# Optimization experiments

Hardware: AMD Instinct MI355X
Metric: run time of the kernel (lower is better)

The kernel has to match this reference:

```python
import jax, jax.numpy as jnp
import numpy as np

ALPHA, BETA, GAMMA, DELTA, EPSILON = 1.0, 0.15, 0.05, 0.0, 0.1
C1 = (0.01 * 255.0) ** 2
C2 = (0.03 * 255.0) ** 2


def _gaussian_kernel11():
    # cv2.getGaussianKernel(11, 1.5) outer product
    g = np.exp(-((np.arange(11) - 5.0) ** 2) / (2.0 * 1.5 ** 2))
    g = g / g.sum()
    return jnp.asarray(np.outer(g, g), dtype=jnp.float32)


def _to_uint8_float(x):
    # clamp to [-1,1], map to [0,1], scale to 255, uint8 truncation (floor)
    x = jnp.clip(x, -1.0, 1.0)
    x01 = jnp.clip((x + 1.0) * 0.5, 0.0, 1.0)
    return jnp.floor(jnp.clip(x01 * 255.0, 0.0, 255.0))


def _depthwise_valid_conv(x, kern2d):
    # x: [B,C,H,W]; 11x11 gaussian, VALID padding == filter2D + [5:-5,5:-5] crop
    C = x.shape[1]
    k = jnp.broadcast_to(kern2d[None, None], (C, 1, 11, 11))
    return jax.lax.conv_general_dilated(
        x, k, window_strides=(1, 1), padding='VALID',
        dimension_numbers=('NCHW', 'OIHW', 'NCHW'), feature_group_count=C)


def _ssim_per_image(img1, img2):
    # img1/img2: [B,C,H,W] floats in [0,255]; basicsr-style SSIM per channel, mean over C
    kern = _gaussian_kernel11()
    conv = lambda t: _depthwise_valid_conv(t, kern)
    mu1, mu2 = conv(img1), conv(img2)
    mu1_sq, mu2_sq, mu1_mu2 = mu1 * mu1, mu2 * mu2, mu1 * mu2
    sigma1_sq = conv(img1 * img1) - mu1_sq
    sigma2_sq = conv(img2 * img2) - mu2_sq
    sigma12 = conv(img1 * img2) - mu1_mu2
    ssim_map = ((2.0 * mu1_mu2 + C1) * (2.0 * sigma12 + C2)) / (
        (mu1_sq + mu2_sq + C1) * (sigma1_sq + sigma2_sq + C2))
    return jnp.mean(ssim_map, axis=(1, 2, 3))  # [B]


def _psnr_per_image(img1, img2):
    mse = jnp.mean((img1 - img2) ** 2, axis=(1, 2, 3))
    psnr = 10.0 * jnp.log10((255.0 ** 2) / jnp.maximum(mse, 1e-12))
    return jnp.where(mse == 0.0, 100.0, psnr)


def setup_inputs() -> dict:
    key = jax.random.key(0)
    k1, k2 = jax.random.split(key)
    shape = (4, 1, 2048, 2048)
    pred = jax.random.normal(k1, shape, dtype=jnp.float32) * 0.5
    target = jax.random.normal(k2, shape, dtype=jnp.float32) * 0.5
    return {"pred": pred, "target": target}


def reference(pred, target):
    # L1 loss
    l1 = jnp.mean(jnp.abs(pred - target))

    # edge-aware gradient loss (finite differences along H and W)
    gx = lambda t: t[:, :, :-1, :] - t[:, :, 1:, :]
    gy = lambda t: t[:, :, :, :-1] - t[:, :, :, 1:]
    grad_loss = (jnp.mean(jnp.abs(gx(pred) - gx(target))) +
                 jnp.mean(jnp.abs(gy(pred) - gy(target))))

    # physical consistency: per-image/channel mean & unbiased std stats + range penalty
    pm = jnp.mean(pred, axis=(2, 3))
    tm = jnp.mean(target, axis=(2, 3))
    energy = jnp.mean((pm - tm) ** 2)
    n = pred.shape[2] * pred.shape[3]
    ps = jnp.sqrt(jnp.sum((pred - pm[:, :, None, None]) ** 2, axis=(2, 3)) / (n - 1))
    ts = jnp.sqrt(jnp.sum((target - tm[:, :, None, None]) ** 2, axis=(2, 3)) / (n - 1))
    dist = jnp.mean((ps - ts) ** 2)
    range_pen = jnp.mean(jax.nn.relu(jnp.abs(pred) - 1.0))
    phys = energy + 0.5 * dist + 0.1 * range_pen

    # SSIM / PSNR on uint8-quantized [0,255] images (metric path, no gradient)
    p8 = _to_uint8_float(pred)
    t8 = _to_uint8_float(target)
    ssim_mean = jnp.clip(jnp.mean(_ssim_per_image(p8, t8)), 0.0, 1.0)
    psnr_mean = jnp.mean(_psnr_per_image(p8, t8))
    ssim_loss = 1.0 - ssim_mean

    total = (ALPHA * l1 + BETA * grad_loss + GAMMA * phys +
             EPSILON * jax.lax.stop_gradient(ssim_loss))
    return total, psnr_mean, ssim_mean
```

## Files before the change

### kernel.cpp

```cpp
#include <hip/hip_runtime.h>
#include <math.h>

#define HDIM 2048
#define WDIM 2048
#define NPIX (HDIM*WDIM)
#define OUTW 2038

#define C1F 6.5025f
#define C2F 58.5225f

constexpr int TH   = 64, TW = 32;
constexpr int IN_R = 80;
constexpr int IQ_S = 56;
constexpr int IQ_H = IN_R * IQ_S;
constexpr int HT_R = 80;
constexpr int HT_A = 32 * HT_R;
constexpr int NCH  = 4;
constexpr int NBLK = 8192;

struct GaussW { float g[11]; };

typedef _Float16 half8 __attribute__((ext_vector_type(8)));
typedef float    f32x4 __attribute__((ext_vector_type(4)));
typedef float    f32x2 __attribute__((ext_vector_type(2)));

__device__ __forceinline__ float quant_u8f(float x) {
    float c = __builtin_amdgcn_fmed3f(x, -1.0f, 1.0f);
    return truncf((c + 1.0f) * 127.5f);
}

__device__ __forceinline__ f32x2 quant2(f32x2 x) {
    f32x2 c = { __builtin_amdgcn_fmed3f(x.x, -1.0f, 1.0f),
                __builtin_amdgcn_fmed3f(x.y, -1.0f, 1.0f) };
    f32x2 v = (c + 1.0f) * 127.5f;
    return { truncf(v.x), truncf(v.y) };
}

__device__ __forceinline__ unsigned pk2(float a, float b) {
    return __builtin_bit_cast(unsigned, __builtin_amdgcn_cvt_pkrtz(a, b));
}

__global__ __launch_bounds__(256, 7) void amsr2_fused(
        const float* __restrict__ pred, const float* __restrict__ targ,
        float* __restrict__ pr, GaussW gw)
{
    __shared__ alignas(16) _Float16 Ubuf[NCH * HT_A];
    __shared__ float sred[16][10];
    _Float16* Iq = Ubuf;
    _Float16* Tg = Ubuf + 2 * IQ_H;

    const int b  = blockIdx.z;
    const int r0 = blockIdx.y * TH;
    const int c0 = blockIdx.x * TW;
    const float* pb = pred + (size_t)b * NPIX;
    const float* tb = targ + (size_t)b * NPIX;
    const bool interior = (blockIdx.y < 31) && (blockIdx.x < 63);

    if (threadIdx.x < 16) {
        int n = threadIdx.x;
#pragma unroll
        for (int i = 0; i < 16; ++i) ((unsigned*)Tg)[n * 16 + i] = 0u;
#pragma unroll
        for (int j = 0; j < 11; ++j) Tg[n * 32 + n + j] = (_Float16)gw.g[j];
    }

    float s0 = 0.f, s1 = 0.f, s2 = 0.f, s3 = 0.f, ssum = 0.f;
    f32x2 s4v = {0.f, 0.f}, s5v = {0.f, 0.f}, s6v = {0.f, 0.f},
          s7v = {0.f, 0.f}, s8v = {0.f, 0.f}, ssv = {0.f, 0.f};

    if (interior) {
#pragma unroll
        for (int i = 0; i < 2; ++i) {
            int item = threadIdx.x + i * 256;
            int r = item >> 3, d = item & 7;
            const float* prow = pb + (size_t)(r0 + r) * WDIM + (c0 + d * 4);
            const float* trow = tb + (size_t)(r0 + r) * WDIM + (c0 + d * 4);
            float4 a4 = *(const float4*)prow;
            float4 b4 = *(const float4*)trow;
            float4 ad = *(const float4*)(prow + WDIM);
            float4 bd = *(const float4*)(trow + WDIM);
            float p5 = prow[4], t5 = trow[4];

            f32x2 a01 = {a4.x, a4.y}, a23 = {a4.z, a4.w};
            f32x2 b01 = {b4.x, b4.y}, b23 = {b4.z, b4.w};
            f32x2 dd01 = a01 - b01, dd23 = a23 - b23;
            float dd4 = p5 - t5;
            f32x2 g01 = f32x2{ad.x, ad.y} - f32x2{bd.x, bd.y};
            f32x2 g23 = f32x2{ad.z, ad.w} - f32x2{bd.z, bd.w};

            s0 += fabsf(dd01.x); s0 += fabsf(dd01.y);
            s0 += fabsf(dd23.x); s0 += fabsf(dd23.y);
            s1 += fabsf(dd01.x - g01.x); s1 += fabsf(dd01.y - g01.y);
            s1 += fabsf(dd23.x - g23.x); s1 += fabsf(dd23.y - g23.y);
            s2 += fabsf(dd01.x - dd01.y); s2 += fabsf(dd01.y - dd23.x);
            s2 += fabsf(dd23.x - dd23.y); s2 += fabsf(dd23.y - dd4);
            s3 += fmaxf(fabsf(a4.x) - 1.0f, 0.0f);
            s3 += fmaxf(fabsf(a4.y) - 1.0f, 0.0f);
            s3 += fmaxf(fabsf(a4.z) - 1.0f, 0.0f);
            s3 += fmaxf(fabsf(a4.w) - 1.0f, 0.0f);
            s4v += a01; s4v += a23;
            s5v += b01; s5v += b23;
            s6v += a01 * a01; s6v += a23 * a23;
            s7v += b01 * b01; s7v += b23 * b23;
            f32x2 qp01 = quant2(a01), qp23 = quant2(a23);
            f32x2 qt01 = quant2(b01), qt23 = quant2(b23);
            f32x2 qd01 = qp01 - qt01, qd23 = qp23 - qt23;
            s8v += qd01 * qd01; s8v += qd23 * qd23;

            *(uint2*)&Iq[r * IQ_S + d * 4] =
                make_uint2(pk2(qp01.x, qp01.y), pk2(qp23.x, qp23.y));
            *(uint2*)&Iq[IQ_H + r * IQ_S + d * 4] =
                make_uint2(pk2(qt01.x, qt01.y), pk2(qt23.x, qt23.y));
        }
        {
            int h = threadIdx.x;
            int r = h >> 2, d = 8 + (h & 3);
            const float* prow = pb + (size_t)(r0 + r) * WDIM + (c0 + d * 4);
            const float* trow = tb + (size_t)(r0 + r) * WDIM + (c0 + d * 4);
            float4 a4 = *(const float4*)prow;
            float4 b4 = *(const float4*)trow;
            f32x2 qp01 = quant2(f32x2{a4.x, a4.y}), qp23 = quant2(f32x2{a4.z, a4.w});
            f32x2 qt01 = quant2(f32x2{b4.x, b4.y}), qt23 = quant2(f32x2{b4.z, b4.w});
            *(uint2*)&Iq[r * IQ_S + d * 4] =
                make_uint2(pk2(qp01.x, qp01.y), pk2(qp23.x, qp23.y));
            *(uint2*)&Iq[IQ_H + r * IQ_S + d * 4] =
                make_uint2(pk2(qt01.x, qt01.y), pk2(qt23.x, qt23.y));
        }
        if (threadIdx.x < 192) {
            int h = threadIdx.x;
            int rq = h / 12;
            int r = 64 + rq, d = h - rq * 12;
            const float* prow = pb + (size_t)(r0 + r) * WDIM + (c0 + d * 4);
            const float* trow = tb + (size_t)(r0 + r) * WDIM + (c0 + d * 4);
            float4 a4 = *(const float4*)prow;
            float4 b4 = *(const float4*)trow;
            f32x2 qp01 = quant2(f32x2{a4.x, a4.y}), qp23 = quant2(f32x2{a4.z, a4.w});
            f32x2 qt01 = quant2(f32x2{b4.x, b4.y}), qt23 = quant2(f32x2{b4.z, b4.w});
            *(uint2*)&Iq[r * IQ_S + d * 4] =
                make_uint2(pk2(qp01.x, qp01.y), pk2(qp23.x, qp23.y));
            *(uint2*)&Iq[IQ_H + r * IQ_S + d * 4] =
                make_uint2(pk2(qt01.x, qt01.y), pk2(qt23.x, qt23.y));
        }
    } else {
#pragma unroll
        for (int i = 0; i < 2; ++i) {
            int item = threadIdx.x + i * 256;
            int r = item >> 3, d = item & 7;
            int gr = r0 + r, gc = c0 + d * 4;
            const float* prow = pb + (size_t)gr * WDIM + gc;
            const float* trow = tb + (size_t)gr * WDIM + gc;
            float4 a4 = *(const float4*)prow;
            float4 b4 = *(const float4*)trow;
            bool down = gr < (HDIM - 1);
            bool hasR = (gc + 4) < WDIM;
            float4 z4 = make_float4(0.f, 0.f, 0.f, 0.f);
            float4 ad = down ? *(const float4*)(prow + WDIM) : z4;
            float4 bd = down ? *(const float4*)(trow + WDIM) : z4;
            float p5 = hasR ? prow[4] : 0.0f;
            float t5 = hasR ? trow[4] : 0.0f;
            float pv[4] = {a4.x, a4.y, a4.z, a4.w};
            float tv[4] = {b4.x, b4.y, b4.z, b4.w};
            float pd[4] = {ad.x, ad.y, ad.z, ad.w};
            float td[4] = {bd.x, bd.y, bd.z, bd.w};
            float qp[4], qt[4];
#pragma unroll
            for (int k = 0; k < 4; ++k) { qp[k] = quant_u8f(pv[k]); qt[k] = quant_u8f(tv[k]); }
#pragma unroll
            for (int k = 0; k < 4; ++k) {
                float av = pv[k], bv = tv[k];
                float dd = av - bv;
                s0 += fabsf(dd);
                s3 += fmaxf(fabsf(av) - 1.0f, 0.0f);
                s4v.x += av;  s5v.x += bv;
                s6v.x = fmaf(av, av, s6v.x);
                s7v.x = fmaf(bv, bv, s7v.x);
                if (down) s1 += fabsf(dd - (pd[k] - td[k]));
                float nr  = (k < 3) ? pv[k + 1] : p5;
                float nt2 = (k < 3) ? tv[k + 1] : t5;
                if (k < 3 || hasR) s2 += fabsf(dd - (nr - nt2));
                float qd = qp[k] - qt[k];
                s8v.x = fmaf(qd, qd, s8v.x);
            }
            *(uint2*)&Iq[r * IQ_S + d * 4] =
                make_uint2(pk2(qp[0], qp[1]), pk2(qp[2], qp[3]));
            *(uint2*)&Iq[IQ_H + r * IQ_S + d * 4] =
                make_uint2(pk2(qt[0], qt[1]), pk2(qt[2], qt[3]));
        }
#pragma unroll
        for (int ph = 0; ph < 2; ++ph) {
            int r, d;
            bool active = true;
            if (ph == 0) { int h = threadIdx.x; r = h >> 2; d = 8 + (h & 3); }
            else {
                int h = threadIdx.x;
                active = h < 192;
                int rq = h / 12;
                r = 64 + rq; d = h - rq * 12;
            }
            if (active) {
                int gr = r0 + r, gc = c0 + d * 4;
                bool rowok = gr < HDIM;
                const float* prow = pb + (size_t)gr * WDIM + gc;
                const float* trow = tb + (size_t)gr * WDIM + gc;
                float qp[4], qt[4];
                if (rowok && (gc + 3) < WDIM) {
                    float4 a4 = *(const float4*)prow;
                    float4 b4 = *(const float4*)trow;
                    qp[0]=quant_u8f(a4.x); qp[1]=quant_u8f(a4.y); qp[2]=quant_u8f(a4.z); qp[3]=quant_u8f(a4.w);
                    qt[0]=quant_u8f(b4.x); qt[1]=quant_u8f(b4.y); qt[2]=quant_u8f(b4.z); qt[3]=quant_u8f(b4.w);
                } else {
#pragma unroll
                    for (int k = 0; k < 4; ++k) {
                        bool ok = rowok && (gc + k) < WDIM;
                        qp[k] = ok ? quant_u8f(prow[k]) : 0.0f;
                        qt[k] = ok ? quant_u8f(trow[k]) : 0.0f;
                    }
                }
                *(uint2*)&Iq[r * IQ_S + d * 4] =
                    make_uint2(pk2(qp[0], qp[1]), pk2(qp[2], qp[3]));
                *(uint2*)&Iq[IQ_H + r * IQ_S + d * 4] =
                    make_uint2(pk2(qt[0], qt[1]), pk2(qt[2], qt[3]));
            }
        }
    }
    __syncthreads();

    const int lane = threadIdx.x & 63;
    const int wid  = threadIdx.x >> 6;
    const int q    = lane >> 4;
    const int ml   = lane & 15;
    const half8 gfrag = *(const half8*)&Tg[ml * 32 + q * 8];
    const f32x4 zero4 = {0.f, 0.f, 0.f, 0.f};
    const _Float16 hquart = (_Float16)0.25f;

    const int npos = (wid < 2) ? 3 : 2;
    half8 hap[3], hat[3];
#pragma unroll
    for (int i = 0; i < 3; ++i) {
        if (i < npos) {
            int pos = wid + i * 4;
            int rb = (pos >> 1) * 16;
            int cb = pos & 1;
            int base = (rb + ml) * IQ_S + cb * 16 + q * 8;
            hap[i] = *(const half8*)&Iq[base];
            hat[i] = *(const half8*)&Iq[IQ_H + base];
        }
    }
    __syncthreads();

#pragma unroll
    for (int i = 0; i < 3; ++i) {
        if (i < npos) {
            int pos = wid + i * 4;
            int rb = (pos >> 1) * 16;
            int cb = pos & 1;
            const half8 ap = hap[i];
            const half8 at = hat[i];
            half8 m2 = (ap * hquart) * ap;
            m2 = (at * hquart) * at + m2;
            f32x4 d0 = __builtin_amdgcn_mfma_f32_16x16x32_f16(ap,      gfrag, zero4, 0, 0, 0);
            f32x4 d1 = __builtin_amdgcn_mfma_f32_16x16x32_f16(at,      gfrag, zero4, 0, 0, 0);
            f32x4 d2 = __builtin_amdgcn_mfma_f32_16x16x32_f16(m2,      gfrag, zero4, 0, 0, 0);
            f32x4 d3 = __builtin_amdgcn_mfma_f32_16x16x32_f16(ap * at, gfrag, zero4, 0, 0, 0);
            int hb = (cb * 16 + ml) * HT_R + rb + q * 4;
            *(uint2*)&Ubuf[0 * HT_A + hb] = make_uint2(pk2(d0[0], d0[1]), pk2(d0[2], d0[3]));
            *(uint2*)&Ubuf[1 * HT_A + hb] = make_uint2(pk2(d1[0], d1[1]), pk2(d1[2], d1[3]));
            *(uint2*)&Ubuf[2 * HT_A + hb] = make_uint2(pk2(d2[0], d2[1]), pk2(d2[2], d2[3]));
            *(uint2*)&Ubuf[3 * HT_A + hb] = make_uint2(pk2(d3[0], d3[1]), pk2(d3[2], d3[3]));
        }
    }
    __syncthreads();

    const int th_ = min(TH, OUTW - r0);
    const int tw_ = min(TW, OUTW - c0);
    for (int vp = wid; vp < 8; vp += 4) {
        int rb2 = (vp >> 1) * 16;
        int cb2 = vp & 1;
        f32x4 acc[NCH];
#pragma unroll
        for (int arr = 0; arr < NCH; ++arr) {
            const half8 bf = *(const half8*)&Ubuf[arr * HT_A +
                                                  (cb2 * 16 + ml) * HT_R + rb2 + q * 8];
            acc[arr] = __builtin_amdgcn_mfma_f32_16x16x32_f16(gfrag, bf, zero4, 0, 0, 0);
        }
        if (interior) {
#pragma unroll
            for (int pp = 0; pp < 2; ++pp) {
                f32x2 mu1 = {acc[0][2*pp], acc[0][2*pp+1]};
                f32x2 mu2 = {acc[1][2*pp], acc[1][2*pp+1]};
                f32x2 h2  = {acc[2][2*pp], acc[2][2*pp+1]};
                f32x2 h12 = {acc[3][2*pp], acc[3][2*pp+1]};
                f32x2 mu12 = mu1 * mu2, mu1s = mu1 * mu1, mu2s = mu2 * mu2;
                f32x2 sg12 = h12 - mu12;
                f32x2 sgs  = 4.0f * h2 - mu1s - mu2s;
                f32x2 num = (2.0f * mu12 + C1F) * (2.0f * sg12 + C2F);
                f32x2 den = (mu1s + mu2s + C1F) * (sgs + C2F);
                f32x2 rp = { __builtin_amdgcn_rcpf(den.x),
                             __builtin_amdgcn_rcpf(den.y) };
                ssv += num * rp;
            }
        } else {
            int col = cb2 * 16 + ml;
#pragma unroll
            for (int reg = 0; reg < 4; ++reg) {
                int row = rb2 + q * 4 + reg;
                if (row < th_ && col < tw_) {
                    float mu1 = acc[0][reg], mu2 = acc[1][reg];
                    float h2  = acc[2][reg], h12 = acc[3][reg];
                    float mu1s = mu1 * mu1, mu2s = mu2 * mu2, mu12 = mu1 * mu2;
                    float sg12 = h12 - mu12;
                    float sgs  = 4.0f * h2 - mu1s - mu2s;
                    float num = (2.0f * mu12 + C1F) * (2.0f * sg12 + C2F);
                    float den = (mu1s + mu2s + C1F) * (sgs + C2F);
                    ssum += num * __builtin_amdgcn_rcpf(den);
                }
            }
        }
    }

    float st10[10];
    st10[0] = s0; st10[1] = s1; st10[2] = s2; st10[3] = s3;
    st10[4] = s4v.x + s4v.y; st10[5] = s5v.x + s5v.y;
    st10[6] = s6v.x + s6v.y; st10[7] = s7v.x + s7v.y;
    st10[8] = s8v.x + s8v.y; st10[9] = ssum + ssv.x + ssv.y;
#pragma unroll
    for (int c = 0; c < 10; ++c) {
        float v = st10[c];
        v += __shfl_xor(v, 8);
        v += __shfl_xor(v, 4);
        v += __shfl_xor(v, 2);
        v += __shfl_xor(v, 1);
        st10[c] = v;
    }
    if ((lane & 15) == 0) {
        int g = wid * 4 + (lane >> 4);
#pragma unroll
        for (int c = 0; c < 10; ++c) sred[g][c] = st10[c];
    }
    __syncthreads();
    if (threadIdx.x < 10) {
        int c = threadIdx.x;
        float t = 0.0f;
#pragma unroll
        for (int g = 0; g < 16; ++g) t += sred[g][c];
        int bid = ((b * 32) + blockIdx.y) * 64 + blockIdx.x;
        pr[c * NBLK + bid] = t;
    }
}

__global__ __launch_bounds__(256) void amsr2_final(
        const float* __restrict__ pr, float* __restrict__ out)
{
    __shared__ double seg[40];
    int wid = threadIdx.x >> 6, lane = threadIdx.x & 63;
    for (int sidx = wid; sidx < 40; sidx += 4) {
        int c = sidx >> 2, b = sidx & 3;
        const float* base = pr + c * NBLK + b * 2048;
        float4 v[8];
#pragma unroll
        for (int it = 0; it < 8; ++it)
            v[it] = *(const float4*)(base + (it * 64 + lane) * 4);
        double acc = 0.0;
#pragma unroll
        for (int it = 0; it < 8; ++it)
            acc += (double)v[it].x + (double)v[it].y + (double)v[it].z + (double)v[it].w;
        for (int off = 32; off > 0; off >>= 1) acc += __shfl_down(acc, off);
        if (lane == 0) seg[sidx] = acc;
    }
    __syncthreads();
    if (threadIdx.x != 0) return;
    const double n = (double)NPIX;
    double sum0 = 0, sum1 = 0, sum2 = 0, sum3 = 0;
    for (int b = 0; b < 4; ++b) {
        sum0 += seg[0*4+b]; sum1 += seg[1*4+b]; sum2 += seg[2*4+b]; sum3 += seg[3*4+b];
    }
    double l1   = sum0 / (4.0 * n);
    double grad = sum1 / (4.0 * 2047.0 * 2048.0) + sum2 / (4.0 * 2048.0 * 2047.0);
    double energy = 0.0, dist = 0.0, psnr_sum = 0.0, ssim_sum = 0.0;
    for (int b = 0; b < 4; ++b) {
        double Sp  = seg[4*4+b],  St  = seg[5*4+b];
        double Spp = seg[6*4+b],  Stt = seg[7*4+b];
        double Su8 = seg[8*4+b],  Sss = seg[9*4+b];
        double pm = Sp / n, tm = St / n;
        double dm = pm - tm; energy += dm * dm;
        double vp = (Spp - n * pm * pm) / (n - 1.0);
        double vt = (Stt - n * tm * tm) / (n - 1.0);
        double ps = sqrt(fmax(vp, 0.0)), ts = sqrt(fmax(vt, 0.0));
        double dd = ps - ts; dist += dd * dd;
        double mse = Su8 / n;
        double psnr = (mse == 0.0) ? 100.0 : 10.0 * log10(65025.0 / fmax(mse, 1e-12));
        psnr_sum += psnr;
        ssim_sum += Sss / ((double)OUTW * (double)OUTW);
    }
    energy *= 0.25; dist *= 0.25;
    double range_pen = sum3 / (4.0 * n);
    double phys = energy + 0.5 * dist + 0.1 * range_pen;
    double ssim_mean = fmin(fmax(ssim_sum * 0.25, 0.0), 1.0);
    double total = l1 + 0.15 * grad + 0.05 * phys + 0.1 * (1.0 - ssim_mean);
    out[0] = (float)total;
    out[1] = (float)(psnr_sum * 0.25);
    out[2] = (float)ssim_mean;
}

extern "C" void kernel_launch(void* const* d_in, const int* in_sizes, int n_in,
                              void* d_out, int out_size, void* d_ws, size_t ws_size,
                              hipStream_t stream)
{
    (void)in_sizes; (void)n_in; (void)out_size; (void)ws_size;
    const float* pred = (const float*)d_in[0];
    const float* targ = (const float*)d_in[1];
    float* out = (float*)d_out;
    float* pr  = (float*)d_ws;

    GaussW gw;
    {
        double e[11], sm = 0.0;
        for (int i = 0; i < 11; ++i) {
            double d = (double)(i - 5);
            e[i] = exp(-(d * d) / 4.5);
            sm += e[i];
        }
        for (int i = 0; i < 11; ++i) gw.g[i] = (float)(e[i] / sm);
    }

    amsr2_fused<<<dim3(64, 32, 4), 256, 0, stream>>>(pred, targ, pr, gw);
    amsr2_final<<<1, 256, 0, stream>>>(pr, out);
}
```

Before: 178.1 us.

## Split fused kernel into streaming stats pass and uint8-staged MFMA SSIM conv

Replaces the single fused tile kernel with a streaming pass that reads pred/target once in column strips, accumulates all loss statistics (reusing the previous row for vertical gradients), and writes uint8-quantized images to workspace. A second kernel reads the compact uint8 halo tiles and runs the separable Gaussian via MFMA to compute the SSIM sum. The aim is to avoid redundant float halo reads and lighten the fused kernel. The cost is an extra global write and read of 32 MB of quantized data plus an extra launch. When the workspace is too small it falls back to the old path.

```diff
diff --git a/kernel.cpp b/kernel.cpp
--- a/kernel.cpp
+++ b/kernel.cpp
@@ -10,12 +10,17 @@
 #define C2F 58.5225f
 
 constexpr int TH   = 64, TW = 32;
-constexpr int IN_R = 80;
-constexpr int IQ_S = 56;
-constexpr int IQ_H = IN_R * IQ_S;
 constexpr int HT_R = 80;
 constexpr int HT_A = 32 * HT_R;
 constexpr int NCH  = 4;
+constexpr int NBLK2 = 8192;
+constexpr int PR9  = 9 * 1024;
+constexpr size_t QBYTES = (size_t)8 * NPIX;
+constexpr size_t WS_NEEDED = QBYTES + (size_t)(PR9 + NBLK2) * 4;
+
+constexpr int IQ_S = 56;
+constexpr int IN_R = 80;
+constexpr int IQ_H = IN_R * IQ_S;
 constexpr int NBLK = 8192;
 
 struct GaussW { float g[11]; };
@@ -28,19 +33,332 @@
     float c = __builtin_amdgcn_fmed3f(x, -1.0f, 1.0f);
     return truncf((c + 1.0f) * 127.5f);
 }
-
 __device__ __forceinline__ f32x2 quant2(f32x2 x) {
     f32x2 c = { __builtin_amdgcn_fmed3f(x.x, -1.0f, 1.0f),
                 __builtin_amdgcn_fmed3f(x.y, -1.0f, 1.0f) };
     f32x2 v = (c + 1.0f) * 127.5f;
     return { truncf(v.x), truncf(v.y) };
 }
-
 __device__ __forceinline__ unsigned pk2(float a, float b) {
     return __builtin_bit_cast(unsigned, __builtin_amdgcn_cvt_pkrtz(a, b));
 }
-
-__global__ __launch_bounds__(256, 7) void amsr2_fused(
+__device__ __forceinline__ unsigned pack4_u8(const float* v) {
+#if __has_builtin(__builtin_amdgcn_cvt_pk_u8_f32)
+    unsigned r = 0;
+    r = __builtin_amdgcn_cvt_pk_u8_f32(v[0], 0, r);
+    r = __builtin_amdgcn_cvt_pk_u8_f32(v[1], 1, r);
+    r = __builtin_amdgcn_cvt_pk_u8_f32(v[2], 2, r);
+    r = __builtin_amdgcn_cvt_pk_u8_f32(v[3], 3, r);
+    return r;
+#else
+    return ((unsigned)(int)v[0]) | (((unsigned)(int)v[1]) << 8) |
+           (((unsigned)(int)v[2]) << 16) | (((unsigned)(int)v[3]) << 24);
+#endif
+}
+__device__ __forceinline__ half8 unpack_u8x8(unsigned lo, unsigned hi) {
+    union { unsigned u[4]; half8 h; } r;
+    r.u[0] = pk2((float)(lo & 0xffu),         (float)((lo >> 8)  & 0xffu));
+    r.u[1] = pk2((float)((lo >> 16) & 0xffu), (float)((lo >> 24) & 0xffu));
+    r.u[2] = pk2((float)(hi & 0xffu),         (float)((hi >> 8)  & 0xffu));
+    r.u[3] = pk2((float)((hi >> 16) & 0xffu), (float)((hi >> 24) & 0xffu));
+    return r.h;
+}
+
+__global__ __launch_bounds__(256, 6) void amsr2_stream(
+        const float* __restrict__ pred, const float* __restrict__ targ,
+        unsigned char* __restrict__ qbuf, float* __restrict__ pr)
+{
+    __shared__ float sred[16][9];
+    const int g   = blockIdx.x * 256 + threadIdx.x;
+    const int b   = g >> 16;
+    const int rem = g & 65535;
+    const int seg = rem >> 9;
+    const int cg  = rem & 511;
+    const int r_start = seg * 16;
+    const bool hasR = (cg != 511);
+
+    const float* pp = pred + (size_t)b * NPIX + (size_t)r_start * WDIM + cg * 4;
+    const float* tt = targ + (size_t)b * NPIX + (size_t)r_start * WDIM + cg * 4;
+    unsigned char* qo = qbuf + (size_t)(b * 2) * NPIX + (size_t)r_start * WDIM + cg * 4;
+
+    float s0 = 0.f, s1 = 0.f, s2 = 0.f, s3 = 0.f;
+    f32x2 s4v = {0,0}, s5v = {0,0}, s6v = {0,0}, s7v = {0,0}, s8v = {0,0};
+    f32x2 pd01 = {0,0}, pd23 = {0,0};
+
+#pragma unroll 4
+    for (int it = 0; it < 16; ++it) {
+        float4 a4 = *(const float4*)pp;
+        float4 b4 = *(const float4*)tt;
+        float p5 = 0.f, t5 = 0.f;
+        if (hasR) { p5 = pp[4]; t5 = tt[4]; }
+
+        f32x2 a01 = {a4.x, a4.y}, a23 = {a4.z, a4.w};
+        f32x2 b01 = {b4.x, b4.y}, b23 = {b4.z, b4.w};
+        f32x2 dd01 = a01 - b01, dd23 = a23 - b23;
+        float dd4 = p5 - t5;
+
+        s0 += fabsf(dd01.x); s0 += fabsf(dd01.y);
+        s0 += fabsf(dd23.x); s0 += fabsf(dd23.y);
+        if (it > 0) {
+            s1 += fabsf(pd01.x - dd01.x); s1 += fabsf(pd01.y - dd01.y);
+            s1 += fabsf(pd23.x - dd23.x); s1 += fabsf(pd23.y - dd23.y);
+        }
+        s2 += fabsf(dd01.x - dd01.y); s2 += fabsf(dd01.y - dd23.x);
+        s2 += fabsf(dd23.x - dd23.y);
+        if (hasR) s2 += fabsf(dd23.y - dd4);
+        s3 += fmaxf(fabsf(a4.x) - 1.0f, 0.0f);
+        s3 += fmaxf(fabsf(a4.y) - 1.0f, 0.0f);
+        s3 += fmaxf(fabsf(a4.z) - 1.0f, 0.0f);
+        s3 += fmaxf(fabsf(a4.w) - 1.0f, 0.0f);
+        s4v += a01; s4v += a23;
+        s5v += b01; s5v += b23;
+        s6v += a01 * a01; s6v += a23 * a23;
+        s7v += b01 * b01; s7v += b23 * b23;
+        f32x2 qp01 = quant2(a01), qp23 = quant2(a23);
+        f32x2 qt01 = quant2(b01), qt23 = quant2(b23);
+        f32x2 qd01 = qp01 - qt01, qd23 = qp23 - qt23;
+        s8v += qd01 * qd01; s8v += qd23 * qd23;
+        float qpv[4] = {qp01.x, qp01.y, qp23.x, qp23.y};
+        float qtv[4] = {qt01.x, qt01.y, qt23.x, qt23.y};
+        *(unsigned*)qo          = pack4_u8(qpv);
+        *(unsigned*)(qo + NPIX) = pack4_u8(qtv);
+
+        pd01 = dd01; pd23 = dd23;
+        pp += WDIM; tt += WDIM; qo += WDIM;
+    }
+    if (seg != 127) {
+        float4 a4 = *(const float4*)pp;
+        float4 b4 = *(const float4*)tt;
+        f32x2 dd01 = f32x2{a4.x, a4.y} - f32x2{b4.x, b4.y};
+        f32x2 dd23 = f32x2{a4.z, a4.w} - f32x2{b4.z, b4.w};
+        s1 += fabsf(pd01.x - dd01.x); s1 += fabsf(pd01.y - dd01.y);
+        s1 += fabsf(pd23.x - dd23.x); s1 += fabsf(pd23.y - dd23.y);
+    }
+
+    const int lane = threadIdx.x & 63;
+    const int wid  = threadIdx.x >> 6;
+    float st9[9] = {s0, s1, s2, s3,
+                    s4v.x + s4v.y, s5v.x + s5v.y,
+                    s6v.x + s6v.y, s7v.x + s7v.y, s8v.x + s8v.y};
+#pragma unroll
+    for (int c = 0; c < 9; ++c) {
+        float v = st9[c];
+        v += __shfl_xor(v, 8);
+        v += __shfl_xor(v, 4);
+        v += __shfl_xor(v, 2);
+        v += __shfl_xor(v, 1);
+        st9[c] = v;
+    }
+    if ((lane & 15) == 0) {
+        int gi = wid * 4 + (lane >> 4);
+#pragma unroll
+        for (int c = 0; c < 9; ++c) sred[gi][c] = st9[c];
+    }
+    __syncthreads();
+    if (threadIdx.x < 9) {
+        int c = threadIdx.x;
+        float t = 0.0f;
+#pragma unroll
+        for (int gi = 0; gi < 16; ++gi) t += sred[gi][c];
+        pr[c * 1024 + blockIdx.x] = t;
+    }
+}
+
+__global__ __launch_bounds__(256, 6) void amsr2_conv(
+        const unsigned char* __restrict__ qbuf, float* __restrict__ pr, GaussW gw)
+{
+    __shared__ alignas(16) _Float16 HT[NCH * HT_A];
+    __shared__ alignas(16) _Float16 Tg[16 * 32];
+    __shared__ float sredS[16];
+
+    const int b  = blockIdx.z;
+    const int r0 = blockIdx.y * TH;
+    const int c0 = blockIdx.x * TW;
+    const bool interior = (blockIdx.y < 31) && (blockIdx.x < 63);
+    const unsigned char* qb0 = qbuf + (size_t)(b * 2) * NPIX;
+
+    if (threadIdx.x < 16) {
+        int n = threadIdx.x;
+#pragma unroll
+        for (int i = 0; i < 16; ++i) ((unsigned*)Tg)[n * 16 + i] = 0u;
+#pragma unroll
+        for (int j = 0; j < 11; ++j) Tg[n * 32 + n + j] = (_Float16)gw.g[j];
+    }
+
+    const int lane = threadIdx.x & 63;
+    const int wid  = threadIdx.x >> 6;
+    const int q    = lane >> 4;
+    const int ml   = lane & 15;
+    const f32x4 zero4 = {0.f, 0.f, 0.f, 0.f};
+    const _Float16 hquart = (_Float16)0.25f;
+
+    const int npos = (wid < 2) ? 3 : 2;
+    uint2 fp[3], ft[3];
+#pragma unroll
+    for (int i = 0; i < 3; ++i) {
+        if (i < npos) {
+            int pos = wid + i * 4;
+            int rb = (pos >> 1) * 16;
+            int cb = pos & 1;
+            int gr = r0 + rb + ml;       if (gr > HDIM - 1) gr = HDIM - 1;
+            int gc = c0 + cb * 16 + q * 8; if (gc > WDIM - 8) gc = WDIM - 8;
+            size_t off = (size_t)gr * WDIM + gc;
+            fp[i] = *(const uint2*)(qb0 + off);
+            ft[i] = *(const uint2*)(qb0 + NPIX + off);
+        }
+    }
+    __syncthreads();
+
+    const half8 gfrag = *(const half8*)&Tg[ml * 32 + q * 8];
+
+#pragma unroll
+    for (int i = 0; i < 3; ++i) {
+        if (i < npos) {
+            int pos = wid + i * 4;
+            int rb = (pos >> 1) * 16;
+            int cb = pos & 1;
+            const half8 ap = unpack_u8x8(fp[i].x, fp[i].y);
+            const half8 at = unpack_u8x8(ft[i].x, ft[i].y);
+            half8 m2 = (ap * hquart) * ap;
+            m2 = (at * hquart) * at + m2;
+            f32x4 d0 = __builtin_amdgcn_mfma_f32_16x16x32_f16(ap,      gfrag, zero4, 0, 0, 0);
+            f32x4 d1 = __builtin_amdgcn_mfma_f32_16x16x32_f16(at,      gfrag, zero4, 0, 0, 0);
+            f32x4 d2 = __builtin_amdgcn_mfma_f32_16x16x32_f16(m2,      gfrag, zero4, 0, 0, 0);
+            f32x4 d3 = __builtin_amdgcn_mfma_f32_16x16x32_f16(ap * at, gfrag, zero4, 0, 0, 0);
+            int hb = (cb * 16 + ml) * HT_R + rb + q * 4;
+            *(uint2*)&HT[0 * HT_A + hb] = make_uint2(pk2(d0[0], d0[1]), pk2(d0[2], d0[3]));
+            *(uint2*)&HT[1 * HT_A + hb] = make_uint2(pk2(d1[0], d1[1]), pk2(d1[2], d1[3]));
+            *(uint2*)&HT[2 * HT_A + hb] = make_uint2(pk2(d2[0], d2[1]), pk2(d2[2], d2[3]));
+            *(uint2*)&HT[3 * HT_A + hb] = make_uint2(pk2(d3[0], d3[1]), pk2(d3[2], d3[3]));
+        }
+    }
+    __syncthreads();
+
+    float ssum = 0.0f;
+    f32x2 ssv = {0.f, 0.f};
+    const int th_ = min(TH, OUTW - r0);
+    const int tw_ = min(TW, OUTW - c0);
+    for (int vp = wid; vp < 8; vp += 4) {
+        int rb2 = (vp >> 1) * 16;
+        int cb2 = vp & 1;
+        f32x4 acc[NCH];
+#pragma unroll
+        for (int arr = 0; arr < NCH; ++arr) {
+            const half8 bf = *(const half8*)&HT[arr * HT_A +
+                                               (cb2 * 16 + ml) * HT_R + rb2 + q * 8];
+            acc[arr] = __builtin_amdgcn_mfma_f32_16x16x32_f16(gfrag, bf, zero4, 0, 0, 0);
+        }
+        if (interior) {
+#pragma unroll
+            for (int pp = 0; pp < 2; ++pp) {
+                f32x2 mu1 = {acc[0][2*pp], acc[0][2*pp+1]};
+                f32x2 mu2 = {acc[1][2*pp], acc[1][2*pp+1]};
+                f32x2 h2  = {acc[2][2*pp], acc[2][2*pp+1]};
+                f32x2 h12 = {acc[3][2*pp], acc[3][2*pp+1]};
+                f32x2 mu12 = mu1 * mu2, mu1s = mu1 * mu1, mu2s = mu2 * mu2;
+                f32x2 sg12 = h12 - mu12;
+                f32x2 sgs  = 4.0f * h2 - mu1s - mu2s;
+                f32x2 num = (2.0f * mu12 + C1F) * (2.0f * sg12 + C2F);
+                f32x2 den = (mu1s + mu2s + C1F) * (sgs + C2F);
+                f32x2 rp = { __builtin_amdgcn_rcpf(den.x),
+                             __builtin_amdgcn_rcpf(den.y) };
+                ssv += num * rp;
+            }
+        } else {
+            int col = cb2 * 16 + ml;
+#pragma unroll
+            for (int reg = 0; reg < 4; ++reg) {
+                int row = rb2 + q * 4 + reg;
+                if (row < th_ && col < tw_) {
+                    float mu1 = acc[0][reg], mu2 = acc[1][reg];
+                    float h2  = acc[2][reg], h12 = acc[3][reg];
+                    float mu1s = mu1 * mu1, mu2s = mu2 * mu2, mu12 = mu1 * mu2;
+                    float sg12 = h12 - mu12;
+                    float sgs  = 4.0f * h2 - mu1s - mu2s;
+                    float num = (2.0f * mu12 + C1F) * (2.0f * sg12 + C2F);
+                    float den = (mu1s + mu2s + C1F) * (sgs + C2F);
+                    ssum += num * __builtin_amdgcn_rcpf(den);
+                }
+            }
+        }
+    }
+
+    float v = ssum + ssv.x + ssv.y;
+    v += __shfl_xor(v, 8);
+    v += __shfl_xor(v, 4);
+    v += __shfl_xor(v, 2);
+    v += __shfl_xor(v, 1);
+    if ((lane & 15) == 0) sredS[wid * 4 + (lane >> 4)] = v;
+    __syncthreads();
+    if (threadIdx.x == 0) {
+        float t = 0.0f;
+#pragma unroll
+        for (int gi = 0; gi < 16; ++gi) t += sredS[gi];
+        int bid2 = ((b * 32) + blockIdx.y) * 64 + blockIdx.x;
+        pr[PR9 + bid2] = t;
+    }
+}
+
+__global__ __launch_bounds__(256) void amsr2_final2(
+        const float* __restrict__ pr, float* __restrict__ out)
+{
+    __shared__ double seg[40];
+    int wid = threadIdx.x >> 6, lane = threadIdx.x & 63;
+    for (int sidx = wid; sidx < 40; sidx += 4) {
+        double acc = 0.0;
+        if (sidx < 36) {
+            int c = sidx >> 2, bb = sidx & 3;
+            const float* base = pr + c * 1024 + bb * 256;
+            float4 v = *(const float4*)(base + lane * 4);
+            acc = (double)v.x + (double)v.y + (double)v.z + (double)v.w;
+        } else {
+            int bb = sidx - 36;
+            const float* base = pr + PR9 + bb * 2048;
+#pragma unroll
+            for (int it = 0; it < 8; ++it) {
+                float4 v = *(const float4*)(base + (it * 64 + lane) * 4);
+                acc += (double)v.x + (double)v.y + (double)v.z + (double)v.w;
+            }
+        }
+        for (int off = 32; off > 0; off >>= 1) acc += __shfl_down(acc, off);
+        if (lane == 0) seg[sidx] = acc;
+    }
+    __syncthreads();
+    if (threadIdx.x != 0) return;
+    const double n = (double)NPIX;
+    double sum0 = 0, sum1 = 0, sum2 = 0, sum3 = 0;
+    for (int b = 0; b < 4; ++b) {
+        sum0 += seg[0*4+b]; sum1 += seg[1*4+b]; sum2 += seg[2*4+b]; sum3 += seg[3*4+b];
+    }
+    double l1   = sum0 / (4.0 * n);
+    double grad = sum1 / (4.0 * 2047.0 * 2048.0) + sum2 / (4.0 * 2048.0 * 2047.0);
+    double energy = 0.0, dist = 0.0, psnr_sum = 0.0, ssim_sum = 0.0;
+    for (int b = 0; b < 4; ++b) {
+        double Sp  = seg[4*4+b],  St  = seg[5*4+b];
+        double Spp = seg[6*4+b],  Stt = seg[7*4+b];
+        double Su8 = seg[8*4+b],  Sss = seg[36+b];
+        double pm = Sp / n, tm = St / n;
+        double dm = pm - tm; energy += dm * dm;
+        double vp = (Spp - n * pm * pm) / (n - 1.0);
+        double vt = (Stt - n * tm * tm) / (n - 1.0);
+        double ps = sqrt(fmax(vp, 0.0)), ts = sqrt(fmax(vt, 0.0));
+        double dd = ps - ts; dist += dd * dd;
+        double mse = Su8 / n;
+        double psnr = (mse == 0.0) ? 100.0 : 10.0 * log10(65025.0 / fmax(mse, 1e-12));
+        psnr_sum += psnr;
+        ssim_sum += Sss / ((double)OUTW * (double)OUTW);
+    }
+    energy *= 0.25; dist *= 0.25;
+    double range_pen = sum3 / (4.0 * n);
+    double phys = energy + 0.5 * dist + 0.1 * range_pen;
+    double ssim_mean = fmin(fmax(ssim_sum * 0.25, 0.0), 1.0);
+    double total = l1 + 0.15 * grad + 0.05 * phys + 0.1 * (1.0 - ssim_mean);
+    out[0] = (float)total;
+    out[1] = (float)(psnr_sum * 0.25);
+    out[2] = (float)ssim_mean;
+}
+
+__global__ __launch_bounds__(256, 7) void amsr2_fused_fb(
         const float* __restrict__ pred, const float* __restrict__ targ,
         float* __restrict__ pr, GaussW gw)
 {
@@ -65,8 +383,7 @@
     }
 
     float s0 = 0.f, s1 = 0.f, s2 = 0.f, s3 = 0.f, ssum = 0.f;
-    f32x2 s4v = {0.f, 0.f}, s5v = {0.f, 0.f}, s6v = {0.f, 0.f},
-          s7v = {0.f, 0.f}, s8v = {0.f, 0.f}, ssv = {0.f, 0.f};
+    f32x2 s4v = {0,0}, s5v = {0,0}, s6v = {0,0}, s7v = {0,0}, s8v = {0,0}, ssv = {0,0};
 
     if (interior) {
 #pragma unroll
@@ -80,14 +397,12 @@
             float4 ad = *(const float4*)(prow + WDIM);
             float4 bd = *(const float4*)(trow + WDIM);
             float p5 = prow[4], t5 = trow[4];
-
             f32x2 a01 = {a4.x, a4.y}, a23 = {a4.z, a4.w};
             f32x2 b01 = {b4.x, b4.y}, b23 = {b4.z, b4.w};
             f32x2 dd01 = a01 - b01, dd23 = a23 - b23;
             float dd4 = p5 - t5;
             f32x2 g01 = f32x2{ad.x, ad.y} - f32x2{bd.x, bd.y};
             f32x2 g23 = f32x2{ad.z, ad.w} - f32x2{bd.z, bd.w};
-
             s0 += fabsf(dd01.x); s0 += fabsf(dd01.y);
             s0 += fabsf(dd23.x); s0 += fabsf(dd23.y);
             s1 += fabsf(dd01.x - g01.x); s1 += fabsf(dd01.y - g01.y);
@@ -106,7 +421,6 @@
             f32x2 qt01 = quant2(b01), qt23 = quant2(b23);
             f32x2 qd01 = qp01 - qt01, qd23 = qp23 - qt23;
             s8v += qd01 * qd01; s8v += qd23 * qd23;
-
             *(uint2*)&Iq[r * IQ_S + d * 4] =
                 make_uint2(pk2(qp01.x, qp01.y), pk2(qp23.x, qp23.y));
             *(uint2*)&Iq[IQ_H + r * IQ_S + d * 4] =
@@ -348,7 +662,7 @@
     }
 }
 
-__global__ __launch_bounds__(256) void amsr2_final(
+__global__ __launch_bounds__(256) void amsr2_final_fb(
         const float* __restrict__ pr, float* __restrict__ out)
 {
     __shared__ double seg[40];
@@ -406,11 +720,10 @@
                               void* d_out, int out_size, void* d_ws, size_t ws_size,
                               hipStream_t stream)
 {
-    (void)in_sizes; (void)n_in; (void)out_size; (void)ws_size;
+    (void)in_sizes; (void)n_in; (void)out_size;
     const float* pred = (const float*)d_in[0];
     const float* targ = (const float*)d_in[1];
     float* out = (float*)d_out;
-    float* pr  = (float*)d_ws;
 
     GaussW gw;
     {
@@ -423,6 +736,15 @@
         for (int i = 0; i < 11; ++i) gw.g[i] = (float)(e[i] / sm);
     }
 
-    amsr2_fused<<<dim3(64, 32, 4), 256, 0, stream>>>(pred, targ, pr, gw);
-    amsr2_final<<<1, 256, 0, stream>>>(pr, out);
-}
+    if (ws_size >= WS_NEEDED) {
+        unsigned char* qbuf = (unsigned char*)d_ws;
+        float* pr = (float*)((char*)d_ws + QBYTES);
+        amsr2_stream<<<dim3(1024, 1, 1), 256, 0, stream>>>(pred, targ, qbuf, pr);
+        amsr2_conv<<<dim3(64, 32, 4), 256, 0, stream>>>(qbuf, pr, gw);
+        amsr2_final2<<<1, 256, 0, stream>>>(pr, out);
+    } else {
+        float* pr = (float*)d_ws;
+        amsr2_fused_fb<<<dim3(64, 32, 4), 256, 0, stream>>>(pred, targ, pr, gw);
+        amsr2_final_fb<<<1, 256, 0, stream>>>(pr, out);
+    }
+}
```

Result: slower. 203.0 us (+13.9%).

## Stage fp32 input tiles into LDS via global_load_lds and quantize from LDS

Applied to the files above, without the earlier changes.

Input tiles for pred and target, including the 11x11 halo, are copied straight from global memory into an fp32 LDS staging buffer with global_load_lds. All statistics and the fp16 quantization for the MFMA convolution are then computed from LDS. Clamped row and column indices replace the separate interior and boundary load paths, which removes branchy per-element global loads and the duplicate neighbour loads. In exchange, the fp32 staging buffer takes more LDS, so the occupancy hint drops from 7 to 5 blocks per CU, and quantization moves after the barrier.

```diff
diff --git a/kernel.cpp b/kernel.cpp
--- a/kernel.cpp
+++ b/kernel.cpp
@@ -10,9 +10,9 @@
 #define C2F 58.5225f
 
 constexpr int TH   = 64, TW = 32;
-constexpr int IN_R = 80;
-constexpr int IQ_S = 56;
-constexpr int IQ_H = IN_R * IQ_S;
+constexpr int S_ROWS = 80;
+constexpr int S_CDW  = 48;
+constexpr int S_IMG  = S_ROWS * S_CDW;
 constexpr int HT_R = 80;
 constexpr int HT_A = 32 * HT_R;
 constexpr int NCH  = 4;
@@ -24,30 +24,47 @@
 typedef float    f32x4 __attribute__((ext_vector_type(4)));
 typedef float    f32x2 __attribute__((ext_vector_type(2)));
 
+#define GLDS16(gp, lp) \
+    __builtin_amdgcn_global_load_lds( \
+        (const __attribute__((address_space(1))) void*)(gp), \
+        (__attribute__((address_space(3))) void*)(lp), 16, 0, 0)
+
 __device__ __forceinline__ float quant_u8f(float x) {
     float c = __builtin_amdgcn_fmed3f(x, -1.0f, 1.0f);
     return truncf((c + 1.0f) * 127.5f);
 }
-
 __device__ __forceinline__ f32x2 quant2(f32x2 x) {
     f32x2 c = { __builtin_amdgcn_fmed3f(x.x, -1.0f, 1.0f),
                 __builtin_amdgcn_fmed3f(x.y, -1.0f, 1.0f) };
     f32x2 v = (c + 1.0f) * 127.5f;
     return { truncf(v.x), truncf(v.y) };
 }
-
 __device__ __forceinline__ unsigned pk2(float a, float b) {
     return __builtin_bit_cast(unsigned, __builtin_amdgcn_cvt_pkrtz(a, b));
 }
-
-__global__ __launch_bounds__(256, 7) void amsr2_fused(
+__device__ __forceinline__ half8 quant8(float4 lo, float4 hi) {
+    union { unsigned u[4]; half8 h; } r;
+    r.u[0] = pk2(quant_u8f(lo.x), quant_u8f(lo.y));
+    r.u[1] = pk2(quant_u8f(lo.z), quant_u8f(lo.w));
+    r.u[2] = pk2(quant_u8f(hi.x), quant_u8f(hi.y));
+    r.u[3] = pk2(quant_u8f(hi.z), quant_u8f(hi.w));
+    return r.h;
+}
+
+__global__ __launch_bounds__(256, 5) void amsr2_fused(
         const float* __restrict__ pred, const float* __restrict__ targ,
         float* __restrict__ pr, GaussW gw)
 {
-    __shared__ alignas(16) _Float16 Ubuf[NCH * HT_A];
+    __shared__ alignas(16) float Stg[2 * S_IMG];
+    __shared__ alignas(16) _Float16 Tg[16 * 32];
     __shared__ float sred[16][10];
-    _Float16* Iq = Ubuf;
-    _Float16* Tg = Ubuf + 2 * IQ_H;
+    _Float16* HTp = (_Float16*)Stg;
+
+    const int tid  = threadIdx.x;
+    const int lane = tid & 63;
+    const int wid  = tid >> 6;
+    const int q    = lane >> 4;
+    const int ml   = lane & 15;
 
     const int b  = blockIdx.z;
     const int r0 = blockIdx.y * TH;
@@ -55,184 +72,80 @@
     const float* pb = pred + (size_t)b * NPIX;
     const float* tb = targ + (size_t)b * NPIX;
     const bool interior = (blockIdx.y < 31) && (blockIdx.x < 63);
-
-    if (threadIdx.x < 16) {
-        int n = threadIdx.x;
+    const bool lastcol  = (blockIdx.x == 63);
+
+    if (tid < 16) {
+        int n = tid;
 #pragma unroll
         for (int i = 0; i < 16; ++i) ((unsigned*)Tg)[n * 16 + i] = 0u;
 #pragma unroll
         for (int j = 0; j < 11; ++j) Tg[n * 32 + n + j] = (_Float16)gw.g[j];
     }
 
+#pragma unroll
+    for (int j = 0; j < 8; ++j) {
+        if (j < 7 || tid < 128) {
+            int item = j * 256 + tid;
+            int img  = item >= 960 ? 1 : 0;
+            int wi   = item - img * 960;
+            int row  = wi / 12;
+            int c16  = wi - row * 12;
+            int gr = r0 + row; if (gr > HDIM - 1) gr = HDIM - 1;
+            int gc = c0 + c16 * 4; if (gc > WDIM - 4) gc = WDIM - 4;
+            const float* gp = (img ? tb : pb) + (size_t)gr * WDIM + gc;
+            unsigned lofs = (unsigned)(j * 256 + (tid & ~63)) * 16u;
+            GLDS16(gp, (char*)Stg + lofs);
+        }
+    }
+    asm volatile("s_waitcnt vmcnt(0)" ::: "memory");
+    __syncthreads();
+
     float s0 = 0.f, s1 = 0.f, s2 = 0.f, s3 = 0.f, ssum = 0.f;
-    f32x2 s4v = {0.f, 0.f}, s5v = {0.f, 0.f}, s6v = {0.f, 0.f},
-          s7v = {0.f, 0.f}, s8v = {0.f, 0.f}, ssv = {0.f, 0.f};
-
-    if (interior) {
-#pragma unroll
-        for (int i = 0; i < 2; ++i) {
-            int item = threadIdx.x + i * 256;
-            int r = item >> 3, d = item & 7;
-            const float* prow = pb + (size_t)(r0 + r) * WDIM + (c0 + d * 4);
-            const float* trow = tb + (size_t)(r0 + r) * WDIM + (c0 + d * 4);
-            float4 a4 = *(const float4*)prow;
-            float4 b4 = *(const float4*)trow;
-            float4 ad = *(const float4*)(prow + WDIM);
-            float4 bd = *(const float4*)(trow + WDIM);
-            float p5 = prow[4], t5 = trow[4];
-
-            f32x2 a01 = {a4.x, a4.y}, a23 = {a4.z, a4.w};
-            f32x2 b01 = {b4.x, b4.y}, b23 = {b4.z, b4.w};
-            f32x2 dd01 = a01 - b01, dd23 = a23 - b23;
-            float dd4 = p5 - t5;
-            f32x2 g01 = f32x2{ad.x, ad.y} - f32x2{bd.x, bd.y};
-            f32x2 g23 = f32x2{ad.z, ad.w} - f32x2{bd.z, bd.w};
-
-            s0 += fabsf(dd01.x); s0 += fabsf(dd01.y);
-            s0 += fabsf(dd23.x); s0 += fabsf(dd23.y);
-            s1 += fabsf(dd01.x - g01.x); s1 += fabsf(dd01.y - g01.y);
-            s1 += fabsf(dd23.x - g23.x); s1 += fabsf(dd23.y - g23.y);
-            s2 += fabsf(dd01.x - dd01.y); s2 += fabsf(dd01.y - dd23.x);
-            s2 += fabsf(dd23.x - dd23.y); s2 += fabsf(dd23.y - dd4);
-            s3 += fmaxf(fabsf(a4.x) - 1.0f, 0.0f);
-            s3 += fmaxf(fabsf(a4.y) - 1.0f, 0.0f);
-            s3 += fmaxf(fabsf(a4.z) - 1.0f, 0.0f);
-            s3 += fmaxf(fabsf(a4.w) - 1.0f, 0.0f);
-            s4v += a01; s4v += a23;
-            s5v += b01; s5v += b23;
-            s6v += a01 * a01; s6v += a23 * a23;
-            s7v += b01 * b01; s7v += b23 * b23;
-            f32x2 qp01 = quant2(a01), qp23 = quant2(a23);
-            f32x2 qt01 = quant2(b01), qt23 = quant2(b23);
-            f32x2 qd01 = qp01 - qt01, qd23 = qp23 - qt23;
-            s8v += qd01 * qd01; s8v += qd23 * qd23;
-
-            *(uint2*)&Iq[r * IQ_S + d * 4] =
-                make_uint2(pk2(qp01.x, qp01.y), pk2(qp23.x, qp23.y));
-            *(uint2*)&Iq[IQ_H + r * IQ_S + d * 4] =
-                make_uint2(pk2(qt01.x, qt01.y), pk2(qt23.x, qt23.y));
-        }
-        {
-            int h = threadIdx.x;
-            int r = h >> 2, d = 8 + (h & 3);
-            const float* prow = pb + (size_t)(r0 + r) * WDIM + (c0 + d * 4);
-            const float* trow = tb + (size_t)(r0 + r) * WDIM + (c0 + d * 4);
-            float4 a4 = *(const float4*)prow;
-            float4 b4 = *(const float4*)trow;
-            f32x2 qp01 = quant2(f32x2{a4.x, a4.y}), qp23 = quant2(f32x2{a4.z, a4.w});
-            f32x2 qt01 = quant2(f32x2{b4.x, b4.y}), qt23 = quant2(f32x2{b4.z, b4.w});
-            *(uint2*)&Iq[r * IQ_S + d * 4] =
-                make_uint2(pk2(qp01.x, qp01.y), pk2(qp23.x, qp23.y));
-            *(uint2*)&Iq[IQ_H + r * IQ_S + d * 4] =
-                make_uint2(pk2(qt01.x, qt01.y), pk2(qt23.x, qt23.y));
-        }
-        if (threadIdx.x < 192) {
-            int h = threadIdx.x;
-            int rq = h / 12;
-            int r = 64 + rq, d = h - rq * 12;
-            const float* prow = pb + (size_t)(r0 + r) * WDIM + (c0 + d * 4);
-            const float* trow = tb + (size_t)(r0 + r) * WDIM + (c0 + d * 4);
-            float4 a4 = *(const float4*)prow;
-            float4 b4 = *(const float4*)trow;
-            f32x2 qp01 = quant2(f32x2{a4.x, a4.y}), qp23 = quant2(f32x2{a4.z, a4.w});
-            f32x2 qt01 = quant2(f32x2{b4.x, b4.y}), qt23 = quant2(f32x2{b4.z, b4.w});
-            *(uint2*)&Iq[r * IQ_S + d * 4] =
-                make_uint2(pk2(qp01.x, qp01.y), pk2(qp23.x, qp23.y));
-            *(uint2*)&Iq[IQ_H + r * IQ_S + d * 4] =
-                make_uint2(pk2(qt01.x, qt01.y), pk2(qt23.x, qt23.y));
-        }
-    } else {
-#pragma unroll
-        for (int i = 0; i < 2; ++i) {
-            int item = threadIdx.x + i * 256;
-            int r = item >> 3, d = item & 7;
-            int gr = r0 + r, gc = c0 + d * 4;
-            const float* prow = pb + (size_t)gr * WDIM + gc;
-            const float* trow = tb + (size_t)gr * WDIM + gc;
-            float4 a4 = *(const float4*)prow;
-            float4 b4 = *(const float4*)trow;
-            bool down = gr < (HDIM - 1);
-            bool hasR = (gc + 4) < WDIM;
-            float4 z4 = make_float4(0.f, 0.f, 0.f, 0.f);
-            float4 ad = down ? *(const float4*)(prow + WDIM) : z4;
-            float4 bd = down ? *(const float4*)(trow + WDIM) : z4;
-            float p5 = hasR ? prow[4] : 0.0f;
-            float t5 = hasR ? trow[4] : 0.0f;
-            float pv[4] = {a4.x, a4.y, a4.z, a4.w};
-            float tv[4] = {b4.x, b4.y, b4.z, b4.w};
-            float pd[4] = {ad.x, ad.y, ad.z, ad.w};
-            float td[4] = {bd.x, bd.y, bd.z, bd.w};
-            float qp[4], qt[4];
-#pragma unroll
-            for (int k = 0; k < 4; ++k) { qp[k] = quant_u8f(pv[k]); qt[k] = quant_u8f(tv[k]); }
-#pragma unroll
-            for (int k = 0; k < 4; ++k) {
-                float av = pv[k], bv = tv[k];
-                float dd = av - bv;
-                s0 += fabsf(dd);
-                s3 += fmaxf(fabsf(av) - 1.0f, 0.0f);
-                s4v.x += av;  s5v.x += bv;
-                s6v.x = fmaf(av, av, s6v.x);
-                s7v.x = fmaf(bv, bv, s7v.x);
-                if (down) s1 += fabsf(dd - (pd[k] - td[k]));
-                float nr  = (k < 3) ? pv[k + 1] : p5;
-                float nt2 = (k < 3) ? tv[k + 1] : t5;
-                if (k < 3 || hasR) s2 += fabsf(dd - (nr - nt2));
-                float qd = qp[k] - qt[k];
-                s8v.x = fmaf(qd, qd, s8v.x);
-            }
-            *(uint2*)&Iq[r * IQ_S + d * 4] =
-                make_uint2(pk2(qp[0], qp[1]), pk2(qp[2], qp[3]));
-            *(uint2*)&Iq[IQ_H + r * IQ_S + d * 4] =
-                make_uint2(pk2(qt[0], qt[1]), pk2(qt[2], qt[3]));
-        }
-#pragma unroll
-        for (int ph = 0; ph < 2; ++ph) {
-            int r, d;
-            bool active = true;
-            if (ph == 0) { int h = threadIdx.x; r = h >> 2; d = 8 + (h & 3); }
-            else {
-                int h = threadIdx.x;
-                active = h < 192;
-                int rq = h / 12;
-                r = 64 + rq; d = h - rq * 12;
-            }
-            if (active) {
-                int gr = r0 + r, gc = c0 + d * 4;
-                bool rowok = gr < HDIM;
-                const float* prow = pb + (size_t)gr * WDIM + gc;
-                const float* trow = tb + (size_t)gr * WDIM + gc;
-                float qp[4], qt[4];
-                if (rowok && (gc + 3) < WDIM) {
-                    float4 a4 = *(const float4*)prow;
-                    float4 b4 = *(const float4*)trow;
-                    qp[0]=quant_u8f(a4.x); qp[1]=quant_u8f(a4.y); qp[2]=quant_u8f(a4.z); qp[3]=quant_u8f(a4.w);
-                    qt[0]=quant_u8f(b4.x); qt[1]=quant_u8f(b4.y); qt[2]=quant_u8f(b4.z); qt[3]=quant_u8f(b4.w);
-                } else {
-#pragma unroll
-                    for (int k = 0; k < 4; ++k) {
-                        bool ok = rowok && (gc + k) < WDIM;
-                        qp[k] = ok ? quant_u8f(prow[k]) : 0.0f;
-                        qt[k] = ok ? quant_u8f(trow[k]) : 0.0f;
-                    }
-                }
-                *(uint2*)&Iq[r * IQ_S + d * 4] =
-                    make_uint2(pk2(qp[0], qp[1]), pk2(qp[2], qp[3]));
-                *(uint2*)&Iq[IQ_H + r * IQ_S + d * 4] =
-                    make_uint2(pk2(qt[0], qt[1]), pk2(qt[2], qt[3]));
-            }
-        }
-    }
-    __syncthreads();
-
-    const int lane = threadIdx.x & 63;
-    const int wid  = threadIdx.x >> 6;
-    const int q    = lane >> 4;
-    const int ml   = lane & 15;
+    f32x2 s4v = {0,0}, s5v = {0,0}, s6v = {0,0},
+          s7v = {0,0}, s8v = {0,0}, ssv = {0,0};
+#pragma unroll
+    for (int i = 0; i < 2; ++i) {
+        int item = tid + i * 256;
+        int r = item >> 3, d = item & 7;
+        const float* pA = &Stg[r * S_CDW + d * 4];
+        const float* pB = &Stg[S_IMG + r * S_CDW + d * 4];
+        float4 a4 = *(const float4*)pA;
+        float4 b4 = *(const float4*)pB;
+        float4 ad = *(const float4*)(pA + S_CDW);
+        float4 bd = *(const float4*)(pB + S_CDW);
+        float p5 = pA[4], t5 = pB[4];
+
+        f32x2 a01 = {a4.x, a4.y}, a23 = {a4.z, a4.w};
+        f32x2 b01 = {b4.x, b4.y}, b23 = {b4.z, b4.w};
+        f32x2 dd01 = a01 - b01, dd23 = a23 - b23;
+        f32x2 g01 = f32x2{ad.x, ad.y} - f32x2{bd.x, bd.y};
+        f32x2 g23 = f32x2{ad.z, ad.w} - f32x2{bd.z, bd.w};
+        bool hasR = !(lastcol && d == 7);
+        float dd4 = hasR ? (p5 - t5) : dd23.y;
+
+        s0 += fabsf(dd01.x); s0 += fabsf(dd01.y);
+        s0 += fabsf(dd23.x); s0 += fabsf(dd23.y);
+        s1 += fabsf(dd01.x - g01.x); s1 += fabsf(dd01.y - g01.y);
+        s1 += fabsf(dd23.x - g23.x); s1 += fabsf(dd23.y - g23.y);
+        s2 += fabsf(dd01.x - dd01.y); s2 += fabsf(dd01.y - dd23.x);
+        s2 += fabsf(dd23.x - dd23.y); s2 += fabsf(dd23.y - dd4);
+        s3 += fmaxf(fabsf(a4.x) - 1.0f, 0.0f);
+        s3 += fmaxf(fabsf(a4.y) - 1.0f, 0.0f);
+        s3 += fmaxf(fabsf(a4.z) - 1.0f, 0.0f);
+        s3 += fmaxf(fabsf(a4.w) - 1.0f, 0.0f);
+        s4v += a01; s4v += a23;
+        s5v += b01; s5v += b23;
+        s6v += a01 * a01; s6v += a23 * a23;
+        s7v += b01 * b01; s7v += b23 * b23;
+        f32x2 qp01 = quant2(a01), qp23 = quant2(a23);
+        f32x2 qt01 = quant2(b01), qt23 = quant2(b23);
+        f32x2 qd01 = qp01 - qt01, qd23 = qp23 - qt23;
+        s8v += qd01 * qd01; s8v += qd23 * qd23;
+    }
+
     const half8 gfrag = *(const half8*)&Tg[ml * 32 + q * 8];
     const f32x4 zero4 = {0.f, 0.f, 0.f, 0.f};
     const _Float16 hquart = (_Float16)0.25f;
-
     const int npos = (wid < 2) ? 3 : 2;
     half8 hap[3], hat[3];
 #pragma unroll
@@ -241,9 +154,13 @@
             int pos = wid + i * 4;
             int rb = (pos >> 1) * 16;
             int cb = pos & 1;
-            int base = (rb + ml) * IQ_S + cb * 16 + q * 8;
-            hap[i] = *(const half8*)&Iq[base];
-            hat[i] = *(const half8*)&Iq[IQ_H + base];
+            int row = rb + ml, cf = cb * 16 + q * 8;
+            const float* pA = &Stg[row * S_CDW + cf];
+            const float* pB = &Stg[S_IMG + row * S_CDW + cf];
+            float4 x0 = *(const float4*)pA, x1 = *(const float4*)(pA + 4);
+            float4 y0 = *(const float4*)pB, y1 = *(const float4*)(pB + 4);
+            hap[i] = quant8(x0, x1);
+            hat[i] = quant8(y0, y1);
         }
     }
     __syncthreads();
@@ -263,10 +180,10 @@
             f32x4 d2 = __builtin_amdgcn_mfma_f32_16x16x32_f16(m2,      gfrag, zero4, 0, 0, 0);
             f32x4 d3 = __builtin_amdgcn_mfma_f32_16x16x32_f16(ap * at, gfrag, zero4, 0, 0, 0);
             int hb = (cb * 16 + ml) * HT_R + rb + q * 4;
-            *(uint2*)&Ubuf[0 * HT_A + hb] = make_uint2(pk2(d0[0], d0[1]), pk2(d0[2], d0[3]));
-            *(uint2*)&Ubuf[1 * HT_A + hb] = make_uint2(pk2(d1[0], d1[1]), pk2(d1[2], d1[3]));
-            *(uint2*)&Ubuf[2 * HT_A + hb] = make_uint2(pk2(d2[0], d2[1]), pk2(d2[2], d2[3]));
-            *(uint2*)&Ubuf[3 * HT_A + hb] = make_uint2(pk2(d3[0], d3[1]), pk2(d3[2], d3[3]));
+            *(uint2*)&HTp[0 * HT_A + hb] = make_uint2(pk2(d0[0], d0[1]), pk2(d0[2], d0[3]));
+            *(uint2*)&HTp[1 * HT_A + hb] = make_uint2(pk2(d1[0], d1[1]), pk2(d1[2], d1[3]));
+            *(uint2*)&HTp[2 * HT_A + hb] = make_uint2(pk2(d2[0], d2[1]), pk2(d2[2], d2[3]));
+            *(uint2*)&HTp[3 * HT_A + hb] = make_uint2(pk2(d3[0], d3[1]), pk2(d3[2], d3[3]));
         }
     }
     __syncthreads();
@@ -279,8 +196,8 @@
         f32x4 acc[NCH];
 #pragma unroll
         for (int arr = 0; arr < NCH; ++arr) {
-            const half8 bf = *(const half8*)&Ubuf[arr * HT_A +
-                                                  (cb2 * 16 + ml) * HT_R + rb2 + q * 8];
+            const half8 bf = *(const half8*)&HTp[arr * HT_A +
+                                                 (cb2 * 16 + ml) * HT_R + rb2 + q * 8];
             acc[arr] = __builtin_amdgcn_mfma_f32_16x16x32_f16(gfrag, bf, zero4, 0, 0, 0);
         }
         if (interior) {
@@ -338,8 +255,8 @@
         for (int c = 0; c < 10; ++c) sred[g][c] = st10[c];
     }
     __syncthreads();
-    if (threadIdx.x < 10) {
-        int c = threadIdx.x;
+    if (tid < 10) {
+        int c = tid;
         float t = 0.0f;
 #pragma unroll
         for (int g = 0; g < 16; ++g) t += sred[g][c];
```

New measurement: 178.4 us. No clear change (+0.1%).
